# Kernel optimization log

Measured on AMD Instinct MI355X. Metric: run time of the kernel, lower is better.

The kernel has to match this reference:

```python
import jax, jax.numpy as jnp
import numpy as np

B, L, S, LA, NA, E, D, H, NHID = 16, 256, 100, 48, 32, 64, 768, 12, 1024
W_IDX = S + 2
EPS = 1e-12


def setup_inputs() -> dict:
    rng = np.random.default_rng(0)
    key = jax.random.key(0)
    ks = jax.random.split(key, 8)
    idxs = np.zeros((B, W_IDX), dtype=np.int64)
    bert_lens = np.zeros((B,), dtype=np.int64)
    is_trig = np.zeros((B, S), dtype=np.float32)
    ent_map = np.zeros((B, S, E), dtype=np.float32)
    argw_mask = np.zeros((B, LA, 1), dtype=np.float32)
    for b in range(B):
        sb = int(rng.integers(60, S + 1))          # n first-subword tokens
        ab = int(rng.integers(8, LA + 1))          # n arg-role subwords
        sent_idx = np.sort(rng.choice(np.arange(1, 2 * sb + 1), size=sb, replace=False))
        sls = 2 * sb + 1                           # second-to-last [SEP] position
        last = sls + ab + 1                        # last [SEP] position
        idxs[b, :sb] = sent_idx
        idxs[b, sb] = sls
        idxs[b, sb + 1] = last
        bert_lens[b] = last + 1
        t0 = int(rng.integers(0, sb - 1))
        is_trig[b, t0:t0 + 2] = 1.0
        eb = int(rng.integers(16, E + 1))
        for e in range(eb):
            ent_map[b, int(rng.integers(0, sb)), e] = 1.0
        argw_mask[b, :ab, 0] = 1.0
    arg_w = np.asarray(jax.random.uniform(ks[0], (B, LA, NA), dtype=jnp.float32)) * argw_mask
    return {
        'all_embeddings': jax.random.normal(ks[1], (B, L, D), dtype=jnp.float32),
        'is_triggers': jnp.asarray(is_trig),
        'arg_weight_matrices': jnp.asarray(arg_w, dtype=jnp.float32),
        'entity_mapping': jnp.asarray(ent_map),
        'att0': jax.random.uniform(ks[2], (B, H, L, L), dtype=jnp.float32),
        'att1': jax.random.uniform(ks[3], (B, H, L, L), dtype=jnp.float32),
        'att2': jax.random.uniform(ks[4], (B, H, L, L), dtype=jnp.float32),
        'W_ta': jax.random.normal(ks[5], (3 * D, D), dtype=jnp.float32) * 0.02,
        'b_ta': jnp.zeros((D,), dtype=jnp.float32),
        'W1': jax.random.normal(ks[6], (6 * D, NHID), dtype=jnp.float32) * 0.02,
        'b1': jnp.zeros((NHID,), dtype=jnp.float32),
        'W2': jax.random.normal(ks[7], (NHID, 1), dtype=jnp.float32) * 0.02,
        'b2': jnp.zeros((1,), dtype=jnp.float32),
        'idxs_to_collect': jnp.asarray(idxs),
        'bert_sentence_lengths': jnp.asarray(bert_lens),
    }


def _l1_normalize(x, axis):
    # F.normalize(x, p=1, dim=axis)
    return x / jnp.clip(jnp.sum(jnp.abs(x), axis=axis, keepdims=True), EPS)


def reference(all_embeddings, is_triggers, arg_weight_matrices, entity_mapping,
              att0, att1, att2, W_ta, b_ta, W1, b1, W2, b2,
              idxs_to_collect, bert_sentence_lengths):
    idxs = idxs_to_collect
    valid = idxs > 0                                   # [B,W]
    n_valid = jnp.sum(valid, axis=1)                   # [B]
    j = jnp.arange(S)
    sent_valid = (j[None, :] < (n_valid - 2)[:, None]).astype(all_embeddings.dtype)  # [B,S]
    sent_idx = idxs[:, :S]
    # first-subword gather, zero-padded (get_fist_subword_embeddings)
    sent_emb = jnp.take_along_axis(all_embeddings, sent_idx[:, :, None], axis=1) * sent_valid[:, :, None]
    # arg-role segment: (second_last_sep+1) .. (bert_len-2), zero-padded to LA
    sls = jnp.take_along_axis(idxs, (n_valid - 2)[:, None], axis=1)[:, 0]   # [B]
    arg_pos = sls[:, None] + 1 + jnp.arange(LA)[None, :]                    # [B,LA]
    arg_valid = (arg_pos < (bert_sentence_lengths - 1)[:, None]).astype(all_embeddings.dtype)
    arg_emb0 = jnp.take_along_axis(all_embeddings, jnp.clip(arg_pos, 0, L - 1)[:, :, None], axis=1) * arg_valid[:, :, None]
    # entity aggregation + trigger mean pooling
    entity = jnp.einsum('bsd,bse->bed', sent_emb, entity_mapping)           # [B,E,D]
    trig = jnp.sum(sent_emb * is_triggers[:, :, None], axis=1) / jnp.sum(is_triggers, axis=1)[:, None]
    arg = jnp.einsum('bld,bla->bad', arg_emb0, arg_weight_matrices)         # [B,NA,D]
    # trigger-aware entity fusion
    trig_e = jnp.broadcast_to(trig[:, None, :], entity.shape)
    nonempty = (jnp.sum(jnp.abs(entity), axis=-1) > 0).astype(entity.dtype)
    ent_cat = jnp.concatenate([entity, trig_e, entity * trig_e], axis=-1)   # [B,E,3D]
    entity = (ent_cat @ W_ta + b_ta) * nonempty[:, :, None]
    # bidirectional token<->arg attention (L1-normalized)
    score = jnp.einsum('bed,bad->bea', entity, arg) / np.sqrt(D)            # [B,E,NA]
    t2a = _l1_normalize(score, 2)[..., None]
    a2t = _l1_normalize(score, 1)[..., None]
    token_argAwared = jnp.sum(arg[:, None] * t2a, axis=2)                   # [B,E,D]
    arg_tokenAwared = jnp.sum(entity[:, :, None] * a2t, axis=1)             # [B,NA,D]
    # select_hidden_att: head-mean, gather collected rows/cols, row-renormalize
    def sel_att(att):
        m = jnp.mean(att, axis=1)                                           # [B,L,L]
        r = jnp.take_along_axis(m, sent_idx[:, :, None], axis=1)            # [B,S,L]
        c = jnp.take_along_axis(r, sent_idx[:, None, :], axis=2)            # [B,S,S]
        c = c * sent_valid[:, :, None] * sent_valid[:, None, :]
        return c / jnp.clip(jnp.sum(c, axis=-1, keepdims=True), EPS)
    t2t = (sel_att(att0) + sel_att(att1) + sel_att(att2)) / 3.0             # [B,S,S]
    a_h2h_tok = t2t @ sent_emb                                              # [B,S,D]
    A_h2h = jnp.einsum('bse,bsd->bed', entity_mapping, a_h2h_tok)           # [B,E,D]
    H_ = jnp.einsum('bse,bsd->bed', entity_mapping, sent_emb)               # [B,E,D]
    a2a = jax.nn.softmax(arg @ jnp.swapaxes(arg, -1, -2), axis=-1)
    A_u2u = a2a @ arg                                                       # [B,NA,D]
    shp = (B, E, NA, D)
    latent = jnp.concatenate([
        jnp.broadcast_to(H_[:, :, None], shp),
        jnp.broadcast_to(arg[:, None], shp),
        jnp.broadcast_to(token_argAwared[:, :, None], shp),
        jnp.broadcast_to(A_h2h[:, :, None], shp),
        jnp.broadcast_to(arg_tokenAwared[:, None], shp),
        jnp.broadcast_to(A_u2u[:, None], shp),
    ], axis=-1)                                                             # [B,E,NA,6D]
    h = jax.nn.gelu(latent @ W1 + b1, approximate=False)
    out = (h @ W2 + b2)[..., 0]                                             # [B,E,NA]
    return out
```

## Files before the change

kernel.cpp:

```cpp
#include <hip/hip_runtime.h>
#include <math.h>

#define B_ 16
#define L_ 256
#define S_ 100
#define LA_ 48
#define NA_ 32
#define E_ 64
#define D_ 768
#define H_ 12
#define NHID_ 1024
#define WIDX_ 102
#define EPSF 1e-12f

typedef __attribute__((ext_vector_type(8))) short s16x8;
typedef __attribute__((ext_vector_type(4))) float f32x4;

__device__ __forceinline__ void split_bf16(float x, unsigned short& h, unsigned short& l) {
  unsigned u = __float_as_uint(x);
  unsigned hr = u + 0x7FFFu + ((u >> 16) & 1u);
  h = (unsigned short)(hr >> 16);
  float r = x - __uint_as_float(hr & 0xFFFF0000u);
  unsigned u2 = __float_as_uint(r);
  unsigned lr = u2 + 0x7FFFu + ((u2 >> 16) & 1u);
  l = (unsigned short)(lr >> 16);
}

__global__ void k_meta(const int* __restrict__ idxs, const int* __restrict__ blen,
                       int* __restrict__ meta) {
  int b = blockIdx.x, t = threadIdx.x;
  __shared__ int cnt;
  if (t == 0) cnt = 0;
  __syncthreads();
  if (t < WIDX_ && idxs[b * WIDX_ + t] > 0) atomicAdd(&cnt, 1);
  __syncthreads();
  if (t == 0) {
    int sb = cnt - 2;
    meta[b * 4 + 0] = sb;
    meta[b * 4 + 1] = idxs[b * WIDX_ + sb];
    meta[b * 4 + 2] = blen[b] - 1;
  }
}

__global__ void k_gather(const float* __restrict__ emb, const int* __restrict__ idxs,
                         const int* __restrict__ meta, float* __restrict__ sent_emb,
                         float* __restrict__ arg_emb) {
  int b = blockIdx.y, y = blockIdx.x, t = threadIdx.x;
  int sb = meta[b * 4 + 0], sls = meta[b * 4 + 1], last = meta[b * 4 + 2];
  if (y < S_) {
    int s = y;
    float* dst = sent_emb + ((size_t)b * S_ + s) * D_;
    if (s < sb) {
      const float* src = emb + ((size_t)b * L_ + idxs[b * WIDX_ + s]) * D_;
      for (int d = t; d < D_; d += 256) dst[d] = src[d];
    } else {
      for (int d = t; d < D_; d += 256) dst[d] = 0.f;
    }
  } else {
    int l = y - S_;
    int pos = sls + 1 + l;
    float* dst = arg_emb + ((size_t)b * LA_ + l) * D_;
    if (pos < last) {
      int p = pos > (L_ - 1) ? (L_ - 1) : pos;
      const float* src = emb + ((size_t)b * L_ + p) * D_;
      for (int d = t; d < D_; d += 256) dst[d] = src[d];
    } else {
      for (int d = t; d < D_; d += 256) dst[d] = 0.f;
    }
  }
}

__global__ void k_trig(const float* __restrict__ sent_emb, const float* __restrict__ is_trig,
                       float* __restrict__ trig) {
  int b = blockIdx.y;
  int d = blockIdx.x * 256 + threadIdx.x;
  float acc = 0.f, den = 0.f;
  for (int s = 0; s < S_; s++) {
    float w = is_trig[b * S_ + s];
    den += w;
    if (w != 0.f) acc += w * sent_emb[((size_t)b * S_ + s) * D_ + d];
  }
  trig[b * D_ + d] = acc / den;
}

__global__ __launch_bounds__(256) void k_entity0(const float* __restrict__ sent_emb,
                                                 const float* __restrict__ ent_map,
                                                 const float* __restrict__ trig,
                                                 unsigned short* __restrict__ e0h,
                                                 unsigned short* __restrict__ e0l,
                                                 unsigned short* __restrict__ e0th,
                                                 unsigned short* __restrict__ e0tl,
                                                 float* __restrict__ ne) {
  int b = blockIdx.y, e = blockIdx.x, t = threadIdx.x;
  float a0 = 0.f, a1 = 0.f, a2 = 0.f;
  for (int s = 0; s < S_; s++) {
    float w = ent_map[((size_t)b * S_ + s) * E_ + e];
    if (w != 0.f) {
      const float* r = sent_emb + ((size_t)b * S_ + s) * D_;
      a0 += w * r[t]; a1 += w * r[t + 256]; a2 += w * r[t + 512];
    }
  }
  size_t o = ((size_t)b * E_ + e) * D_;
  const float* tr = trig + b * D_;
  unsigned short h, lo;
  split_bf16(a0, h, lo); e0h[o + t] = h; e0l[o + t] = lo;
  split_bf16(a1, h, lo); e0h[o + t + 256] = h; e0l[o + t + 256] = lo;
  split_bf16(a2, h, lo); e0h[o + t + 512] = h; e0l[o + t + 512] = lo;
  split_bf16(a0 * tr[t], h, lo); e0th[o + t] = h; e0tl[o + t] = lo;
  split_bf16(a1 * tr[t + 256], h, lo); e0th[o + t + 256] = h; e0tl[o + t + 256] = lo;
  split_bf16(a2 * tr[t + 512], h, lo); e0th[o + t + 512] = h; e0tl[o + t + 512] = lo;
  __shared__ float red[256];
  red[t] = fabsf(a0) + fabsf(a1) + fabsf(a2);
  __syncthreads();
  for (int s2 = 128; s2 > 0; s2 >>= 1) {
    if (t < s2) red[t] += red[t + s2];
    __syncthreads();
  }
  if (t == 0) ne[b * E_ + e] = (red[0] > 0.f) ? 1.f : 0.f;
}

__global__ __launch_bounds__(256) void k_wsum(const float* __restrict__ Wm, int wstride, int sy,
                                              int sx, const float* __restrict__ Vm,
                                              float* __restrict__ Om,
                                              unsigned short* __restrict__ oh,
                                              unsigned short* __restrict__ ol, int Y) {
  int b = blockIdx.y, x = blockIdx.x, t = threadIdx.x;
  float a0 = 0.f, a1 = 0.f, a2 = 0.f;
  const float* wb = Wm + (size_t)b * wstride + (size_t)x * sx;
  const float* vb = Vm + (size_t)b * Y * D_;
  for (int y = 0; y < Y; y++) {
    float w = wb[(size_t)y * sy];
    if (w != 0.f) {
      const float* r = vb + (size_t)y * D_;
      a0 += w * r[t]; a1 += w * r[t + 256]; a2 += w * r[t + 512];
    }
  }
  size_t oidx = ((size_t)b * gridDim.x + x) * D_;
  if (Om) {
    Om[oidx + t] = a0; Om[oidx + t + 256] = a1; Om[oidx + t + 512] = a2;
  }
  if (oh) {
    unsigned short h, lo;
    split_bf16(a0, h, lo); oh[oidx + t] = h; ol[oidx + t] = lo;
    split_bf16(a1, h, lo); oh[oidx + t + 256] = h; ol[oidx + t + 256] = lo;
    split_bf16(a2, h, lo); oh[oidx + t + 512] = h; ol[oidx + t + 512] = lo;
  }
}

__global__ void k_tb(const float* __restrict__ trig, const float* __restrict__ W_ta,
                     const float* __restrict__ b_ta, float* __restrict__ tb) {
  int b = blockIdx.y;
  int d = blockIdx.x * 256 + threadIdx.x;
  float acc0 = b_ta[d], acc1 = 0.f, acc2 = 0.f, acc3 = 0.f;
  float acc4 = 0.f, acc5 = 0.f, acc6 = 0.f, acc7 = 0.f;
  const float* tr = trig + b * D_;
  const float* w = W_ta + (size_t)D_ * D_ + d;
  for (int k = 0; k < D_; k += 8) {
    acc0 += tr[k + 0] * w[(size_t)(k + 0) * D_];
    acc1 += tr[k + 1] * w[(size_t)(k + 1) * D_];
    acc2 += tr[k + 2] * w[(size_t)(k + 2) * D_];
    acc3 += tr[k + 3] * w[(size_t)(k + 3) * D_];
    acc4 += tr[k + 4] * w[(size_t)(k + 4) * D_];
    acc5 += tr[k + 5] * w[(size_t)(k + 5) * D_];
    acc6 += tr[k + 6] * w[(size_t)(k + 6) * D_];
    acc7 += tr[k + 7] * w[(size_t)(k + 7) * D_];
  }
  tb[b * D_ + d] = ((acc0 + acc1) + (acc2 + acc3)) + ((acc4 + acc5) + (acc6 + acc7));
}

__global__ __launch_bounds__(256) void k_cvtT(const float* __restrict__ src, int K, int N,
                                              unsigned short* __restrict__ th,
                                              unsigned short* __restrict__ tl) {
  __shared__ float tile[32][33];
  int k0 = blockIdx.x * 32, n0 = blockIdx.y * 32;
  int tr = threadIdx.x >> 3, c4 = (threadIdx.x & 7) * 4;
  float4 v = *(const float4*)(src + (size_t)(k0 + tr) * N + n0 + c4);
  tile[tr][c4] = v.x; tile[tr][c4 + 1] = v.y; tile[tr][c4 + 2] = v.z; tile[tr][c4 + 3] = v.w;
  __syncthreads();
  unsigned short h[4], l[4];
#pragma unroll
  for (int i = 0; i < 4; ++i) split_bf16(tile[c4 + i][tr], h[i], l[i]);
  size_t oo = (size_t)(n0 + tr) * K + k0 + c4;
  th[oo + 0] = h[0]; th[oo + 1] = h[1]; th[oo + 2] = h[2]; th[oo + 3] = h[3];
  tl[oo + 0] = l[0]; tl[oo + 1] = l[1]; tl[oo + 2] = l[2]; tl[oo + 3] = l[3];
}

__global__ __launch_bounds__(256) void k_mgemm(
    int phase,
    const unsigned short* __restrict__ e0h, const unsigned short* __restrict__ e0l,
    const unsigned short* __restrict__ e0th, const unsigned short* __restrict__ e0tl,
    const unsigned short* __restrict__ Ah2hh, const unsigned short* __restrict__ Ah2hl,
    const unsigned short* __restrict__ argmh, const unsigned short* __restrict__ argml,
    const unsigned short* __restrict__ Au2uh, const unsigned short* __restrict__ Au2ul,
    const unsigned short* __restrict__ tokAh, const unsigned short* __restrict__ tokAl,
    const unsigned short* __restrict__ argTh, const unsigned short* __restrict__ argTl,
    const unsigned short* __restrict__ WtaTh, const unsigned short* __restrict__ WtaTl,
    const unsigned short* __restrict__ W1Th, const unsigned short* __restrict__ W1Tl,
    float* __restrict__ entn, float* __restrict__ PeA, float* __restrict__ PaA,
    float* __restrict__ PeC, float* __restrict__ PaC,
    const float* __restrict__ tb, const float* __restrict__ ne,
    const float* __restrict__ b1) {
  int z = blockIdx.z;
  const unsigned short *A0h_, *A0l_, *A1h_, *A1l_, *Bh_, *Bl_;
  float* C;
  size_t koff0, koff1;
  int bstride, mtiles, niter, N, ep = 0;
  if (phase == 0) {
    if (z == 0) {
      A0h_ = e0h; A0l_ = e0l; A1h_ = e0th; A1l_ = e0tl; Bh_ = WtaTh; Bl_ = WtaTl;
      bstride = 2304; koff0 = 0; koff1 = 1536; C = entn; N = 768; mtiles = 16; niter = 48; ep = 1;
    } else if (z == 1) {
      A0h_ = e0h; A0l_ = e0l; A1h_ = Ah2hh; A1l_ = Ah2hl; Bh_ = W1Th; Bl_ = W1Tl;
      bstride = 4608; koff0 = 0; koff1 = 3 * 768; C = PeA; N = 1024; mtiles = 16; niter = 48;
    } else {
      A0h_ = argmh; A0l_ = argml; A1h_ = Au2uh; A1l_ = Au2ul; Bh_ = W1Th; Bl_ = W1Tl;
      bstride = 4608; koff0 = 768; koff1 = 5 * 768; C = PaA; N = 1024; mtiles = 8; niter = 48;
    }
  } else {
    if (z == 0) {
      A0h_ = tokAh; A0l_ = tokAl; A1h_ = tokAh; A1l_ = tokAl; Bh_ = W1Th; Bl_ = W1Tl;
      bstride = 4608; koff0 = 2 * 768; koff1 = 2 * 768; C = PeC; N = 1024; mtiles = 16;
      niter = 24; ep = 2;
    } else {
      A0h_ = argTh; A0l_ = argTl; A1h_ = argTh; A1l_ = argTl; Bh_ = W1Th; Bl_ = W1Tl;
      bstride = 4608; koff0 = 4 * 768; koff1 = 4 * 768; C = PaC; N = 1024; mtiles = 8;
      niter = 24; ep = 3;
    }
  }
  int bx = blockIdx.x, by = blockIdx.y;
  if (by >= mtiles || bx * 64 >= N) return;

  __shared__ unsigned short As[2][4][64][8];
  __shared__ unsigned short Bs[2][4][64][8];

  int tid = threadIdx.x;
  int srow = tid >> 2, sg = tid & 3;
  size_t aoff = (size_t)(by * 64 + srow) * 768 + sg * 8;
  size_t brow = (size_t)(bx * 64 + srow) * bstride + sg * 8;
  size_t boff0 = brow + koff0, boff1 = brow + koff1;

  s16x8 rAh = *(const s16x8*)(A0h_ + aoff);
  s16x8 rAl = *(const s16x8*)(A0l_ + aoff);
  s16x8 rBh = *(const s16x8*)(Bh_ + boff0);
  s16x8 rBl = *(const s16x8*)(Bl_ + boff0);

  int lane = tid & 63, wave = tid >> 6;
  int wm = wave >> 1, wn = wave & 1;
  int fg = lane >> 4, fr = lane & 15;
  int ar0 = wm * 32 + fr;
  int bc0 = wn * 32 + fr;

  f32x4 acc00 = {0.f, 0.f, 0.f, 0.f}, acc01 = {0.f, 0.f, 0.f, 0.f};
  f32x4 acc10 = {0.f, 0.f, 0.f, 0.f}, acc11 = {0.f, 0.f, 0.f, 0.f};

  for (int it = 0; it < niter; ++it) {
    __syncthreads();
    *(s16x8*)&As[0][sg][srow][0] = rAh;
    *(s16x8*)&As[1][sg][srow][0] = rAl;
    *(s16x8*)&Bs[0][sg][srow][0] = rBh;
    *(s16x8*)&Bs[1][sg][srow][0] = rBl;
    __syncthreads();
    if (it + 1 < niter) {
      int l = it + 1;
      int p = (l >= 24) ? 1 : 0;
      size_t ka = (size_t)(l - (p ? 24 : 0)) * 32;
      rAh = *(const s16x8*)((p ? A1h_ : A0h_) + aoff + ka);
      rAl = *(const s16x8*)((p ? A1l_ : A0l_) + aoff + ka);
      size_t bo = (p ? boff1 : boff0) + ka;
      rBh = *(const s16x8*)(Bh_ + bo);
      rBl = *(const s16x8*)(Bl_ + bo);
    }
    s16x8 ah0 = *(const s16x8*)&As[0][fg][ar0][0];
    s16x8 ah1 = *(const s16x8*)&As[0][fg][ar0 + 16][0];
    s16x8 al0 = *(const s16x8*)&As[1][fg][ar0][0];
    s16x8 al1 = *(const s16x8*)&As[1][fg][ar0 + 16][0];
    s16x8 bh0 = *(const s16x8*)&Bs[0][fg][bc0][0];
    s16x8 bh1 = *(const s16x8*)&Bs[0][fg][bc0 + 16][0];
    s16x8 bl0 = *(const s16x8*)&Bs[1][fg][bc0][0];
    s16x8 bl1 = *(const s16x8*)&Bs[1][fg][bc0 + 16][0];
    acc00 = __builtin_amdgcn_mfma_f32_16x16x32_bf16(ah0, bh0, acc00, 0, 0, 0);
    acc00 = __builtin_amdgcn_mfma_f32_16x16x32_bf16(ah0, bl0, acc00, 0, 0, 0);
    acc00 = __builtin_amdgcn_mfma_f32_16x16x32_bf16(al0, bh0, acc00, 0, 0, 0);
    acc01 = __builtin_amdgcn_mfma_f32_16x16x32_bf16(ah0, bh1, acc01, 0, 0, 0);
    acc01 = __builtin_amdgcn_mfma_f32_16x16x32_bf16(ah0, bl1, acc01, 0, 0, 0);
    acc01 = __builtin_amdgcn_mfma_f32_16x16x32_bf16(al0, bh1, acc01, 0, 0, 0);
    acc10 = __builtin_amdgcn_mfma_f32_16x16x32_bf16(ah1, bh0, acc10, 0, 0, 0);
    acc10 = __builtin_amdgcn_mfma_f32_16x16x32_bf16(ah1, bl0, acc10, 0, 0, 0);
    acc10 = __builtin_amdgcn_mfma_f32_16x16x32_bf16(al1, bh0, acc10, 0, 0, 0);
    acc11 = __builtin_amdgcn_mfma_f32_16x16x32_bf16(ah1, bh1, acc11, 0, 0, 0);
    acc11 = __builtin_amdgcn_mfma_f32_16x16x32_bf16(ah1, bl1, acc11, 0, 0, 0);
    acc11 = __builtin_amdgcn_mfma_f32_16x16x32_bf16(al1, bh1, acc11, 0, 0, 0);
  }

  f32x4 accs[2][2] = {{acc00, acc01}, {acc10, acc11}};
  int colb = bx * 64 + wn * 32 + fr;
  int rowb = by * 64 + wm * 32 + fg * 4;
#pragma unroll
  for (int i = 0; i < 2; ++i) {
#pragma unroll
    for (int j = 0; j < 2; ++j) {
      int col = colb + j * 16;
#pragma unroll
      for (int r = 0; r < 4; ++r) {
        int row = rowb + i * 16 + r;
        float v = accs[i][j][r];
        if (ep == 1) v = (v + tb[(row >> 6) * D_ + col]) * ne[row];
        else if (ep == 2) v = v + PeA[(size_t)row * NHID_ + col] + b1[col];
        else if (ep == 3) v = v + PaA[(size_t)row * NHID_ + col];
        C[(size_t)row * N + col] = v;
      }
    }
  }
}

__global__ __launch_bounds__(256) void k_score(const float* __restrict__ entn,
                                               const float* __restrict__ argm,
                                               float* __restrict__ score) {
  int b = blockIdx.y, e = blockIdx.x, t = threadIdx.x;
  __shared__ float ent[D_];
  const float* er = entn + ((size_t)b * E_ + e) * D_;
  for (int d = t; d < D_; d += 256) ent[d] = er[d];
  __syncthreads();
  int wave = t >> 6, lane = t & 63;
  const float scale = 0.03608439182435161f;
  for (int a = wave; a < NA_; a += 4) {
    const float* ar = argm + ((size_t)b * NA_ + a) * D_;
    float p = 0.f;
#pragma unroll
    for (int i = 0; i < 12; i++) {
      int d = lane + 64 * i;
      p += ent[d] * ar[d];
    }
    for (int off = 32; off > 0; off >>= 1) p += __shfl_down(p, off);
    if (lane == 0) score[((size_t)b * E_ + e) * NA_ + a] = p * scale;
  }
}

__global__ void k_norm(const float* __restrict__ score, float* __restrict__ t2a,
                       float* __restrict__ a2t) {
  int b = blockIdx.x, t = threadIdx.x;
  __shared__ float s[E_ * NA_];
  __shared__ float rs[E_];
  __shared__ float cs[NA_];
  for (int i = t; i < E_ * NA_; i += 256) s[i] = score[(size_t)b * E_ * NA_ + i];
  __syncthreads();
  if (t < E_) {
    float sum = 0.f;
    for (int a = 0; a < NA_; a++) sum += fabsf(s[t * NA_ + a]);
    rs[t] = fmaxf(sum, EPSF);
  } else if (t >= 64 && t < 96) {
    int a = t - 64;
    float sum = 0.f;
    for (int e = 0; e < E_; e++) sum += fabsf(s[e * NA_ + a]);
    cs[a] = fmaxf(sum, EPSF);
  }
  __syncthreads();
  for (int i = t; i < E_ * NA_; i += 256) {
    int e = i >> 5, a = i & 31;
    float v = s[i];
    t2a[(size_t)b * E_ * NA_ + i] = v / rs[e];
    a2t[(size_t)b * E_ * NA_ + i] = v / cs[a];
  }
}

__global__ __launch_bounds__(256) void k_a2a(const float* __restrict__ argm,
                                             float* __restrict__ a2a) {
  int b = blockIdx.y, a = blockIdx.x, t = threadIdx.x;
  __shared__ float sA[D_];
  __shared__ float lg[NA_];
  const float* ar = argm + ((size_t)b * NA_ + a) * D_;
  for (int d = t; d < D_; d += 256) sA[d] = ar[d];
  __syncthreads();
  int wave = t >> 6, lane = t & 63;
  for (int a2 = wave; a2 < NA_; a2 += 4) {
    const float* br = argm + ((size_t)b * NA_ + a2) * D_;
    float p = 0.f;
#pragma unroll
    for (int i = 0; i < 12; i++) {
      int d = lane + 64 * i;
      p += sA[d] * br[d];
    }
    for (int off = 32; off > 0; off >>= 1) p += __shfl_down(p, off);
    if (lane == 0) lg[a2] = p;
  }
  __syncthreads();
  if (t < 64) {
    float v = (t < NA_) ? lg[t] : -INFINITY;
    float m = v;
    for (int mask = 16; mask > 0; mask >>= 1) m = fmaxf(m, __shfl_xor(m, mask));
    float ex = (t < NA_) ? expf(v - m) : 0.f;
    float sm = ex;
    for (int mask = 16; mask > 0; mask >>= 1) sm += __shfl_xor(sm, mask);
    if (t < NA_) a2a[((size_t)b * NA_ + a) * NA_ + t] = ex / sm;
  }
}

__global__ __launch_bounds__(128) void k_t2t(const float* __restrict__ att0,
                                             const float* __restrict__ att1,
                                             const float* __restrict__ att2,
                                             const int* __restrict__ idxs,
                                             const int* __restrict__ meta,
                                             float* __restrict__ t2t) {
  int b = blockIdx.y, s = blockIdx.x, t = threadIdx.x;
  int sb = meta[b * 4 + 0];
  float* out = t2t + ((size_t)b * S_ + s) * S_;
  if (s >= sb) {
    for (int j = t; j < S_; j += 128) out[j] = 0.f;
    return;
  }
  int Is = idxs[b * WIDX_ + s];
  int It = (t < S_) ? idxs[b * WIDX_ + t] : 0;
  __shared__ float row[256];
  __shared__ float red[128];
  const float* atts[3] = {att0, att1, att2};
  float accout = 0.f;
  for (int q = 0; q < 3; q++) {
    float r0 = 0.f, r1 = 0.f;
    const float* base = atts[q] + (((size_t)b * H_) * L_ + Is) * L_;
    for (int h = 0; h < H_; h++) {
      const float* rp = base + (size_t)h * L_ * L_;
      r0 += rp[t];
      r1 += rp[t + 128];
    }
    row[t] = r0;
    row[t + 128] = r1;
    __syncthreads();
    float v = (t < sb) ? row[It] * (1.f / 12.f) : 0.f;
    red[t] = v;
    __syncthreads();
    for (int s2 = 64; s2 > 0; s2 >>= 1) {
      if (t < s2) red[t] += red[t + s2];
      __syncthreads();
    }
    float rsum = red[0];
    __syncthreads();
    accout += v / fmaxf(rsum, EPSF) * (1.f / 3.f);
  }
  if (t < S_) out[t] = accout;
}

__global__ __launch_bounds__(256) void k_final(const float* __restrict__ ps,
                                               const float* __restrict__ qs,
                                               const float* __restrict__ W2,
                                               const float* __restrict__ b2,
                                               float* __restrict__ out) {
  int b = blockIdx.y, e = blockIdx.x, t = threadIdx.x;
  int wave = t >> 6, lane = t & 63;
  const float ks = 0.70710678118654752f;
  size_t po = ((size_t)b * E_ + e) * NHID_ + lane * 4;
  float4 p0 = *(const float4*)(ps + po);
  float4 p1 = *(const float4*)(ps + po + 256);
  float4 p2 = *(const float4*)(ps + po + 512);
  float4 p3 = *(const float4*)(ps + po + 768);
  const float* w2p = W2 + lane * 4;
  float4 w0 = *(const float4*)(w2p);
  float4 w1 = *(const float4*)(w2p + 256);
  float4 w2 = *(const float4*)(w2p + 512);
  float4 w3 = *(const float4*)(w2p + 768);
  __shared__ float outs[NA_];
#pragma unroll 2
  for (int a = wave; a < NA_; a += 4) {
    size_t qo = ((size_t)b * NA_ + a) * NHID_ + lane * 4;
    float4 q0 = *(const float4*)(qs + qo);
    float4 q1 = *(const float4*)(qs + qo + 256);
    float4 q2 = *(const float4*)(qs + qo + 512);
    float4 q3 = *(const float4*)(qs + qo + 768);
    float acc = 0.f;
#define GEL4(pp, qq, ww)                                          \
    {                                                             \
      float x0 = pp.x + qq.x, x1 = pp.y + qq.y;                   \
      float x2 = pp.z + qq.z, x3 = pp.w + qq.w;                   \
      float g0 = 0.5f * x0 * (1.f + erff(x0 * ks));               \
      float g1 = 0.5f * x1 * (1.f + erff(x1 * ks));               \
      float g2 = 0.5f * x2 * (1.f + erff(x2 * ks));               \
      float g3 = 0.5f * x3 * (1.f + erff(x3 * ks));               \
      acc += g0 * ww.x + g1 * ww.y + g2 * ww.z + g3 * ww.w;       \
    }
    GEL4(p0, q0, w0)
    GEL4(p1, q1, w1)
    GEL4(p2, q2, w2)
    GEL4(p3, q3, w3)
#undef GEL4
    acc += __shfl_xor(acc, 32);
    acc += __shfl_xor(acc, 16);
    acc += __shfl_xor(acc, 8);
    acc += __shfl_xor(acc, 4);
    acc += __shfl_xor(acc, 2);
    acc += __shfl_xor(acc, 1);
    if (lane == 0) outs[a] = acc;
  }
  __syncthreads();
  if (t < NA_) out[((size_t)b * E_ + e) * NA_ + t] = outs[t] + b2[0];
}

extern "C" void kernel_launch(void* const* d_in, const int* in_sizes, int n_in,
                              void* d_out, int out_size, void* d_ws, size_t ws_size,
                              hipStream_t stream) {
  const float* emb    = (const float*)d_in[0];
  const float* istrig = (const float*)d_in[1];
  const float* argw   = (const float*)d_in[2];
  const float* entmap = (const float*)d_in[3];
  const float* att0   = (const float*)d_in[4];
  const float* att1   = (const float*)d_in[5];
  const float* att2   = (const float*)d_in[6];
  const float* W_ta   = (const float*)d_in[7];
  const float* b_ta   = (const float*)d_in[8];
  const float* W1     = (const float*)d_in[9];
  const float* b1     = (const float*)d_in[10];
  const float* W2     = (const float*)d_in[11];
  const float* b2     = (const float*)d_in[12];
  const int*   idxs   = (const int*)d_in[13];
  const int*   blen   = (const int*)d_in[14];
  float* out = (float*)d_out;

  float* ws = (float*)d_ws;
  size_t o = 0;
  int* meta = (int*)ws; o += 256;
  float* sent_emb = ws + o; o += (size_t)B_ * S_ * D_;
  float* arg_emb  = ws + o; o += (size_t)B_ * LA_ * D_;
  float* trig     = ws + o; o += (size_t)B_ * D_;
  float* argm     = ws + o; o += (size_t)B_ * NA_ * D_;
  float* entn     = ws + o; o += (size_t)B_ * E_ * D_;
  float* tb       = ws + o; o += (size_t)B_ * D_;
  float* ne       = ws + o; o += (size_t)B_ * E_;
  float* score    = ws + o; o += (size_t)B_ * E_ * NA_;
  float* t2a      = ws + o; o += (size_t)B_ * E_ * NA_;
  float* a2t      = ws + o; o += (size_t)B_ * E_ * NA_;
  float* t2t      = ws + o; o += (size_t)B_ * S_ * S_;
  float* ah2h     = ws + o; o += (size_t)B_ * S_ * D_;
  float* a2a      = ws + o; o += (size_t)B_ * NA_ * NA_;
  float* PeA      = ws + o; o += (size_t)B_ * E_ * NHID_;
  float* PaA      = ws + o; o += (size_t)B_ * NA_ * NHID_;
  float* PeC = sent_emb;
  float* PaC = arg_emb;

  o = (o + 3) & ~(size_t)3;
  unsigned short* us = (unsigned short*)(ws + o);
  size_t uo = 0;
  unsigned short* e0h   = us + uo; uo += (size_t)B_ * E_ * D_;
  unsigned short* e0l   = us + uo; uo += (size_t)B_ * E_ * D_;
  unsigned short* e0th  = us + uo; uo += (size_t)B_ * E_ * D_;
  unsigned short* e0tl  = us + uo; uo += (size_t)B_ * E_ * D_;
  unsigned short* Ah2hh = us + uo; uo += (size_t)B_ * E_ * D_;
  unsigned short* Ah2hl = us + uo; uo += (size_t)B_ * E_ * D_;
  unsigned short* argmh = us + uo; uo += (size_t)B_ * NA_ * D_;
  unsigned short* argml = us + uo; uo += (size_t)B_ * NA_ * D_;
  unsigned short* Au2uh = us + uo; uo += (size_t)B_ * NA_ * D_;
  unsigned short* Au2ul = us + uo; uo += (size_t)B_ * NA_ * D_;
  unsigned short* tokAh = us + uo; uo += (size_t)B_ * E_ * D_;
  unsigned short* tokAl = us + uo; uo += (size_t)B_ * E_ * D_;
  unsigned short* argTh = us + uo; uo += (size_t)B_ * NA_ * D_;
  unsigned short* argTl = us + uo; uo += (size_t)B_ * NA_ * D_;
  unsigned short* WtaTh = us + uo; uo += (size_t)2304 * 768;
  unsigned short* WtaTl = us + uo; uo += (size_t)2304 * 768;
  unsigned short* W1Th  = us + uo; uo += (size_t)4608 * 1024;
  unsigned short* W1Tl  = us + uo; uo += (size_t)4608 * 1024;

  k_meta<<<B_, 128, 0, stream>>>(idxs, blen, meta);
  k_cvtT<<<dim3(2304 / 32, 768 / 32), 256, 0, stream>>>(W_ta, 2304, 768, WtaTh, WtaTl);
  k_cvtT<<<dim3(4608 / 32, 1024 / 32), 256, 0, stream>>>(W1, 4608, 1024, W1Th, W1Tl);
  k_gather<<<dim3(S_ + LA_, B_), 256, 0, stream>>>(emb, idxs, meta, sent_emb, arg_emb);
  k_trig<<<dim3(3, B_), 256, 0, stream>>>(sent_emb, istrig, trig);
  k_entity0<<<dim3(E_, B_), 256, 0, stream>>>(sent_emb, entmap, trig, e0h, e0l, e0th, e0tl, ne);
  k_wsum<<<dim3(NA_, B_), 256, 0, stream>>>(argw, LA_ * NA_, NA_, 1, arg_emb, argm, argmh,
                                            argml, LA_);
  k_tb<<<dim3(3, B_), 256, 0, stream>>>(trig, W_ta, b_ta, tb);
  k_t2t<<<dim3(S_, B_), 128, 0, stream>>>(att0, att1, att2, idxs, meta, t2t);
  k_wsum<<<dim3(S_, B_), 256, 0, stream>>>(t2t, S_ * S_, 1, S_, sent_emb, ah2h, nullptr,
                                           nullptr, S_);
  k_wsum<<<dim3(E_, B_), 256, 0, stream>>>(entmap, S_ * E_, E_, 1, ah2h, nullptr, Ah2hh,
                                           Ah2hl, S_);
  k_a2a<<<dim3(NA_, B_), 256, 0, stream>>>(argm, a2a);
  k_wsum<<<dim3(NA_, B_), 256, 0, stream>>>(a2a, NA_ * NA_, 1, NA_, argm, nullptr, Au2uh,
                                            Au2ul, NA_);

  k_mgemm<<<dim3(16, 16, 3), 256, 0, stream>>>(0, e0h, e0l, e0th, e0tl, Ah2hh, Ah2hl, argmh,
                                               argml, Au2uh, Au2ul, tokAh, tokAl, argTh,
                                               argTl, WtaTh, WtaTl, W1Th, W1Tl, entn, PeA,
                                               PaA, PeC, PaC, tb, ne, b1);

  k_score<<<dim3(E_, B_), 256, 0, stream>>>(entn, argm, score);
  k_norm<<<B_, 256, 0, stream>>>(score, t2a, a2t);
  k_wsum<<<dim3(E_, B_), 256, 0, stream>>>(t2a, E_ * NA_, 1, NA_, argm, nullptr, tokAh,
                                           tokAl, NA_);
  k_wsum<<<dim3(NA_, B_), 256, 0, stream>>>(a2t, E_ * NA_, NA_, 1, entn, nullptr, argTh,
                                            argTl, E_);

  k_mgemm<<<dim3(16, 16, 2), 256, 0, stream>>>(1, e0h, e0l, e0th, e0tl, Ah2hh, Ah2hl, argmh,
                                               argml, Au2uh, Au2ul, tokAh, tokAl, argTh,
                                               argTl, WtaTh, WtaTl, W1Th, W1Tl, entn, PeA,
                                               PaA, PeC, PaC, tb, ne, b1);

  k_final<<<dim3(E_, B_), 256, 0, stream>>>(PeC, PaC, W2, b2, out);
}
```

Measured before the change: 551.6 us.

## Reassociate attention-weighted projections through W1 and swizzle GEMM LDS layout

Matrix associativity is used to project argm and entn through their W1 slices before the attention weights are applied, so (t2a@argm)@W1 becomes t2a@(argm@W1). The argm projection moves into the first GEMM launch and the entn projection runs in its own launch, and a new k_mix kernel applies the t2a/a2t weights and adds the partial sums. This removes the two k_wsum passes and their dependency on the score/norm step before the GEMM. It adds two extra fp32 intermediate buffers, and the reordered summation may change rounding slightly. The LDS tiles are also laid out row-major with an XOR swizzle, aimed at reducing bank conflicts on the fragment reads.

After: 504.9 us. -8.5%, faster.

```diff
diff --git a/kernel.cpp b/kernel.cpp
--- a/kernel.cpp
+++ b/kernel.cpp
@@ -192,19 +192,17 @@
     const unsigned short* __restrict__ Ah2hh, const unsigned short* __restrict__ Ah2hl,
     const unsigned short* __restrict__ argmh, const unsigned short* __restrict__ argml,
     const unsigned short* __restrict__ Au2uh, const unsigned short* __restrict__ Au2ul,
-    const unsigned short* __restrict__ tokAh, const unsigned short* __restrict__ tokAl,
-    const unsigned short* __restrict__ argTh, const unsigned short* __restrict__ argTl,
     const unsigned short* __restrict__ WtaTh, const unsigned short* __restrict__ WtaTl,
     const unsigned short* __restrict__ W1Th, const unsigned short* __restrict__ W1Tl,
-    float* __restrict__ entn, float* __restrict__ PeA, float* __restrict__ PaA,
-    float* __restrict__ PeC, float* __restrict__ PaC,
-    const float* __restrict__ tb, const float* __restrict__ ne,
-    const float* __restrict__ b1) {
+    float* __restrict__ entn, unsigned short* __restrict__ entnh,
+    unsigned short* __restrict__ entnl,
+    float* __restrict__ PeA, float* __restrict__ PaA,
+    float* __restrict__ P2, float* __restrict__ Q2,
+    const float* __restrict__ tb, const float* __restrict__ ne) {
   int z = blockIdx.z;
   const unsigned short *A0h_, *A0l_, *A1h_, *A1l_, *Bh_, *Bl_;
   float* C;
-  size_t koff0, koff1;
-  int bstride, mtiles, niter, N, ep = 0;
+  int koff0, koff1, bstride, mtiles, niter, N, ep = 0;
   if (phase == 0) {
     if (z == 0) {
       A0h_ = e0h; A0l_ = e0l; A1h_ = e0th; A1l_ = e0tl; Bh_ = WtaTh; Bl_ = WtaTl;
@@ -212,29 +210,26 @@
     } else if (z == 1) {
       A0h_ = e0h; A0l_ = e0l; A1h_ = Ah2hh; A1l_ = Ah2hl; Bh_ = W1Th; Bl_ = W1Tl;
       bstride = 4608; koff0 = 0; koff1 = 3 * 768; C = PeA; N = 1024; mtiles = 16; niter = 48;
-    } else {
+    } else if (z == 2) {
       A0h_ = argmh; A0l_ = argml; A1h_ = Au2uh; A1l_ = Au2ul; Bh_ = W1Th; Bl_ = W1Tl;
       bstride = 4608; koff0 = 768; koff1 = 5 * 768; C = PaA; N = 1024; mtiles = 8; niter = 48;
+    } else {
+      A0h_ = argmh; A0l_ = argml; A1h_ = argmh; A1l_ = argml; Bh_ = W1Th; Bl_ = W1Tl;
+      bstride = 4608; koff0 = 2 * 768; koff1 = 2 * 768; C = P2; N = 1024; mtiles = 8; niter = 24;
     }
   } else {
-    if (z == 0) {
-      A0h_ = tokAh; A0l_ = tokAl; A1h_ = tokAh; A1l_ = tokAl; Bh_ = W1Th; Bl_ = W1Tl;
-      bstride = 4608; koff0 = 2 * 768; koff1 = 2 * 768; C = PeC; N = 1024; mtiles = 16;
-      niter = 24; ep = 2;
-    } else {
-      A0h_ = argTh; A0l_ = argTl; A1h_ = argTh; A1l_ = argTl; Bh_ = W1Th; Bl_ = W1Tl;
-      bstride = 4608; koff0 = 4 * 768; koff1 = 4 * 768; C = PaC; N = 1024; mtiles = 8;
-      niter = 24; ep = 3;
-    }
+    A0h_ = entnh; A0l_ = entnl; A1h_ = entnh; A1l_ = entnl; Bh_ = W1Th; Bl_ = W1Tl;
+    bstride = 4608; koff0 = 4 * 768; koff1 = 4 * 768; C = Q2; N = 1024; mtiles = 16; niter = 24;
   }
   int bx = blockIdx.x, by = blockIdx.y;
   if (by >= mtiles || bx * 64 >= N) return;
 
-  __shared__ unsigned short As[2][4][64][8];
-  __shared__ unsigned short Bs[2][4][64][8];
+  __shared__ unsigned short As[2][64][4][8];
+  __shared__ unsigned short Bs[2][64][4][8];
 
   int tid = threadIdx.x;
   int srow = tid >> 2, sg = tid & 3;
+  int wc = sg ^ ((srow >> 1) & 3);
   size_t aoff = (size_t)(by * 64 + srow) * 768 + sg * 8;
   size_t brow = (size_t)(bx * 64 + srow) * bstride + sg * 8;
   size_t boff0 = brow + koff0, boff1 = brow + koff1;
@@ -249,16 +244,18 @@
   int fg = lane >> 4, fr = lane & 15;
   int ar0 = wm * 32 + fr;
   int bc0 = wn * 32 + fr;
+  int ca = fg ^ ((ar0 >> 1) & 3);
+  int cb = fg ^ ((bc0 >> 1) & 3);
 
   f32x4 acc00 = {0.f, 0.f, 0.f, 0.f}, acc01 = {0.f, 0.f, 0.f, 0.f};
   f32x4 acc10 = {0.f, 0.f, 0.f, 0.f}, acc11 = {0.f, 0.f, 0.f, 0.f};
 
   for (int it = 0; it < niter; ++it) {
     __syncthreads();
-    *(s16x8*)&As[0][sg][srow][0] = rAh;
-    *(s16x8*)&As[1][sg][srow][0] = rAl;
-    *(s16x8*)&Bs[0][sg][srow][0] = rBh;
-    *(s16x8*)&Bs[1][sg][srow][0] = rBl;
+    *(s16x8*)&As[0][srow][wc][0] = rAh;
+    *(s16x8*)&As[1][srow][wc][0] = rAl;
+    *(s16x8*)&Bs[0][srow][wc][0] = rBh;
+    *(s16x8*)&Bs[1][srow][wc][0] = rBl;
     __syncthreads();
     if (it + 1 < niter) {
       int l = it + 1;
@@ -270,14 +267,14 @@
       rBh = *(const s16x8*)(Bh_ + bo);
       rBl = *(const s16x8*)(Bl_ + bo);
     }
-    s16x8 ah0 = *(const s16x8*)&As[0][fg][ar0][0];
-    s16x8 ah1 = *(const s16x8*)&As[0][fg][ar0 + 16][0];
-    s16x8 al0 = *(const s16x8*)&As[1][fg][ar0][0];
-    s16x8 al1 = *(const s16x8*)&As[1][fg][ar0 + 16][0];
-    s16x8 bh0 = *(const s16x8*)&Bs[0][fg][bc0][0];
-    s16x8 bh1 = *(const s16x8*)&Bs[0][fg][bc0 + 16][0];
-    s16x8 bl0 = *(const s16x8*)&Bs[1][fg][bc0][0];
-    s16x8 bl1 = *(const s16x8*)&Bs[1][fg][bc0 + 16][0];
+    s16x8 ah0 = *(const s16x8*)&As[0][ar0][ca][0];
+    s16x8 ah1 = *(const s16x8*)&As[0][ar0 + 16][ca][0];
+    s16x8 al0 = *(const s16x8*)&As[1][ar0][ca][0];
+    s16x8 al1 = *(const s16x8*)&As[1][ar0 + 16][ca][0];
+    s16x8 bh0 = *(const s16x8*)&Bs[0][bc0][cb][0];
+    s16x8 bh1 = *(const s16x8*)&Bs[0][bc0 + 16][cb][0];
+    s16x8 bl0 = *(const s16x8*)&Bs[1][bc0][cb][0];
+    s16x8 bl1 = *(const s16x8*)&Bs[1][bc0 + 16][cb][0];
     acc00 = __builtin_amdgcn_mfma_f32_16x16x32_bf16(ah0, bh0, acc00, 0, 0, 0);
     acc00 = __builtin_amdgcn_mfma_f32_16x16x32_bf16(ah0, bl0, acc00, 0, 0, 0);
     acc00 = __builtin_amdgcn_mfma_f32_16x16x32_bf16(al0, bh0, acc00, 0, 0, 0);
@@ -304,9 +301,13 @@
       for (int r = 0; r < 4; ++r) {
         int row = rowb + i * 16 + r;
         float v = accs[i][j][r];
-        if (ep == 1) v = (v + tb[(row >> 6) * D_ + col]) * ne[row];
-        else if (ep == 2) v = v + PeA[(size_t)row * NHID_ + col] + b1[col];
-        else if (ep == 3) v = v + PaA[(size_t)row * NHID_ + col];
+        if (ep == 1) {
+          v = (v + tb[(row >> 6) * D_ + col]) * ne[row];
+          unsigned short hh, ll;
+          split_bf16(v, hh, ll);
+          entnh[(size_t)row * D_ + col] = hh;
+          entnl[(size_t)row * D_ + col] = ll;
+        }
         C[(size_t)row * N + col] = v;
       }
     }
@@ -437,6 +438,50 @@
     accout += v / fmaxf(rsum, EPSF) * (1.f / 3.f);
   }
   if (t < S_) out[t] = accout;
+}
+
+__global__ __launch_bounds__(256) void k_mix(const float* __restrict__ PeA,
+                                             const float* __restrict__ PaA,
+                                             const float* __restrict__ P2,
+                                             const float* __restrict__ Q2,
+                                             const float* __restrict__ t2a,
+                                             const float* __restrict__ a2t,
+                                             const float* __restrict__ b1,
+                                             float* __restrict__ ps, float* __restrict__ qs) {
+  int b = blockIdx.y, x = blockIdx.x, t = threadIdx.x;
+  int n0 = t * 4;
+  __shared__ float w[E_];
+  if (x < E_) {
+    int e = x;
+    size_t ro = ((size_t)b * E_ + e) * NHID_ + n0;
+    float4 acc = *(const float4*)(PeA + ro);
+    float4 bb = *(const float4*)(b1 + n0);
+    acc.x += bb.x; acc.y += bb.y; acc.z += bb.z; acc.w += bb.w;
+    if (t < NA_) w[t] = t2a[((size_t)b * E_ + e) * NA_ + t];
+    __syncthreads();
+    const float* pb = P2 + (size_t)b * NA_ * NHID_ + n0;
+#pragma unroll 4
+    for (int a = 0; a < NA_; a++) {
+      float ww = w[a];
+      float4 p = *(const float4*)(pb + (size_t)a * NHID_);
+      acc.x += ww * p.x; acc.y += ww * p.y; acc.z += ww * p.z; acc.w += ww * p.w;
+    }
+    *(float4*)(ps + ro) = acc;
+  } else {
+    int a = x - E_;
+    size_t ro = ((size_t)b * NA_ + a) * NHID_ + n0;
+    float4 acc = *(const float4*)(PaA + ro);
+    for (int i = t; i < E_; i += 256) w[i] = a2t[((size_t)b * E_ + i) * NA_ + a];
+    __syncthreads();
+    const float* qb = Q2 + (size_t)b * E_ * NHID_ + n0;
+#pragma unroll 4
+    for (int e = 0; e < E_; e++) {
+      float ww = w[e];
+      float4 q = *(const float4*)(qb + (size_t)e * NHID_);
+      acc.x += ww * q.x; acc.y += ww * q.y; acc.z += ww * q.z; acc.w += ww * q.w;
+    }
+    *(float4*)(qs + ro) = acc;
+  }
 }
 
 __global__ __launch_bounds__(256) void k_final(const float* __restrict__ ps,
@@ -531,8 +576,10 @@
   float* a2a      = ws + o; o += (size_t)B_ * NA_ * NA_;
   float* PeA      = ws + o; o += (size_t)B_ * E_ * NHID_;
   float* PaA      = ws + o; o += (size_t)B_ * NA_ * NHID_;
-  float* PeC = sent_emb;
-  float* PaC = arg_emb;
+  float* P2       = ws + o; o += (size_t)B_ * NA_ * NHID_;
+  float* Q2       = ws + o; o += (size_t)B_ * E_ * NHID_;
+  float* ps = sent_emb;
+  float* qs = arg_emb;
 
   o = (o + 3) & ~(size_t)3;
   unsigned short* us = (unsigned short*)(ws + o);
@@ -547,10 +594,8 @@
   unsigned short* argml = us + uo; uo += (size_t)B_ * NA_ * D_;
   unsigned short* Au2uh = us + uo; uo += (size_t)B_ * NA_ * D_;
   unsigned short* Au2ul = us + uo; uo += (size_t)B_ * NA_ * D_;
-  unsigned short* tokAh = us + uo; uo += (size_t)B_ * E_ * D_;
-  unsigned short* tokAl = us + uo; uo += (size_t)B_ * E_ * D_;
-  unsigned short* argTh = us + uo; uo += (size_t)B_ * NA_ * D_;
-  unsigned short* argTl = us + uo; uo += (size_t)B_ * NA_ * D_;
+  unsigned short* entnh = us + uo; uo += (size_t)B_ * E_ * D_;
+  unsigned short* entnl = us + uo; uo += (size_t)B_ * E_ * D_;
   unsigned short* WtaTh = us + uo; uo += (size_t)2304 * 768;
   unsigned short* WtaTl = us + uo; uo += (size_t)2304 * 768;
   unsigned short* W1Th  = us + uo; uo += (size_t)4608 * 1024;
@@ -574,22 +619,17 @@
   k_wsum<<<dim3(NA_, B_), 256, 0, stream>>>(a2a, NA_ * NA_, 1, NA_, argm, nullptr, Au2uh,
                                             Au2ul, NA_);
 
-  k_mgemm<<<dim3(16, 16, 3), 256, 0, stream>>>(0, e0h, e0l, e0th, e0tl, Ah2hh, Ah2hl, argmh,
-                                               argml, Au2uh, Au2ul, tokAh, tokAl, argTh,
-                                               argTl, WtaTh, WtaTl, W1Th, W1Tl, entn, PeA,
-                                               PaA, PeC, PaC, tb, ne, b1);
+  k_mgemm<<<dim3(16, 16, 4), 256, 0, stream>>>(0, e0h, e0l, e0th, e0tl, Ah2hh, Ah2hl, argmh,
+                                               argml, Au2uh, Au2ul, WtaTh, WtaTl, W1Th, W1Tl,
+                                               entn, entnh, entnl, PeA, PaA, P2, Q2, tb, ne);
+
+  k_mgemm<<<dim3(16, 16, 1), 256, 0, stream>>>(1, e0h, e0l, e0th, e0tl, Ah2hh, Ah2hl, argmh,
+                                               argml, Au2uh, Au2ul, WtaTh, WtaTl, W1Th, W1Tl,
+                                               entn, entnh, entnl, PeA, PaA, P2, Q2, tb, ne);
 
   k_score<<<dim3(E_, B_), 256, 0, stream>>>(entn, argm, score);
   k_norm<<<B_, 256, 0, stream>>>(score, t2a, a2t);
-  k_wsum<<<dim3(E_, B_), 256, 0, stream>>>(t2a, E_ * NA_, 1, NA_, argm, nullptr, tokAh,
-                                           tokAl, NA_);
-  k_wsum<<<dim3(NA_, B_), 256, 0, stream>>>(a2t, E_ * NA_, NA_, 1, entn, nullptr, argTh,
-                                            argTl, E_);
-
-  k_mgemm<<<dim3(16, 16, 2), 256, 0, stream>>>(1, e0h, e0l, e0th, e0tl, Ah2hh, Ah2hl, argmh,
-                                               argml, Au2uh, Au2ul, tokAh, tokAl, argTh,
-                                               argTl, WtaTh, WtaTl, W1Th, W1Tl, entn, PeA,
-                                               PaA, PeC, PaC, tb, ne, b1);
-
-  k_final<<<dim3(E_, B_), 256, 0, stream>>>(PeC, PaC, W2, b2, out);
-}
+  k_mix<<<dim3(E_ + NA_, B_), 256, 0, stream>>>(PeA, PaA, P2, Q2, t2a, a2t, b1, ps, qs);
+
+  k_final<<<dim3(E_, B_), 256, 0, stream>>>(ps, qs, W2, b2, out);
+}
```
